# Kernel optimization log

Hardware: AMD Instinct MI355X
Metric: run time of the kernel (lower is better)

## Reference

```python
import jax, jax.numpy as jnp
import numpy as np

HEADS = 8
DIM_HEAD = 64
WINDOW = 128
PERSIST = 4
EPS = 1.1920929e-07  # torch nn.RMSNorm default eps = finfo(fp32).eps


def _rope_freqs(n, d, dtype):
    inv_freq = 1.0 / (10000.0 ** (jnp.arange(0, d, 2, dtype=jnp.float32) / d))
    freqs = jnp.arange(n, dtype=jnp.float32)[:, None] * inv_freq[None, :]  # [n, d/2]
    freqs = jnp.repeat(freqs, 2, axis=-1)  # interleaved repeat -> [n, d]
    return jnp.cos(freqs).astype(dtype), jnp.sin(freqs).astype(dtype)


def _rotate_half(x):
    # interleaved pairs (x0,x1),(x2,x3)... -> (-x1,x0),(-x3,x2)...
    x = x.reshape(*x.shape[:-1], -1, 2)
    x1, x2 = x[..., 0], x[..., 1]
    return jnp.stack((-x2, x1), axis=-1).reshape(*x.shape[:-2], -1)


def setup_inputs() -> dict:
    key = jax.random.key(0)
    k1, k2, k3 = jax.random.split(key, 3)
    B, N, D = 1, 4096, 1024
    dim_inner = HEADS * DIM_HEAD  # 512
    return {
        "seq": jax.random.normal(k1, (B, N, D), dtype=jnp.float32),
        "g": jnp.ones((D,), dtype=jnp.float32),
        "w_qkv": jax.random.normal(k2, (D, 3 * dim_inner), dtype=jnp.float32) * 0.02,
        "w_out": jax.random.normal(k3, (dim_inner, D), dtype=jnp.float32) * 0.02,
    }


def reference(seq, g, w_qkv, w_out):
    B, N, D = seq.shape
    H, Dh = HEADS, DIM_HEAD

    # RMSNorm
    x = seq * jax.lax.rsqrt(jnp.mean(seq * seq, axis=-1, keepdims=True) + EPS) * g

    # QKV projection -> [B, H, N, Dh]
    qkv = x @ w_qkv
    q, k, v = jnp.split(qkv, 3, axis=-1)
    to_heads = lambda t: t.reshape(B, N, H, Dh).transpose(0, 2, 1, 3)
    q, k, v = map(to_heads, (q, k, v))

    # rotary embeddings (same positions for q and k)
    cos, sin = _rope_freqs(N, Dh, q.dtype)
    q = q * cos + _rotate_half(q) * sin
    k = k * cos + _rotate_half(k) * sin

    # causal & (persist | sliding-window) mask
    idx = jnp.arange(N)
    dist = idx[:, None] - idx[None, :]
    mask = (dist >= 0) & ((idx[None, :] < PERSIST) | (dist <= WINDOW))  # [N, N]

    scale = Dh ** -0.5
    scores = jnp.einsum("bhid,bhjd->bhij", q, k) * scale
    neg = -jnp.finfo(scores.dtype).max
    scores = jnp.where(mask[None, None], scores, neg)
    attn = jax.nn.softmax(scores, axis=-1)
    out = jnp.einsum("bhij,bhjd->bhid", attn, v)

    out = out.transpose(0, 2, 1, 3).reshape(B, N, H * Dh)
    return out @ w_out
```

## Files before the change

### kernel.cpp

```cpp
#include <hip/hip_runtime.h>
#include <hip/hip_bf16.h>
#include <math.h>

#define SEQ    4096
#define DMODEL 1024
#define NHEADS 8
#define DH     64
#define DINNER 512
#define NQKV   1536
#define WINDOW 128
#define PERSIST 4
#define EPS 1.1920929e-07f

typedef unsigned short u16;
typedef unsigned int   u32;
typedef __bf16  bf16_8 __attribute__((ext_vector_type(8)));
typedef float   f32x4  __attribute__((ext_vector_type(4)));

union BV { bf16_8 v; u16 s[8]; };

__device__ __forceinline__ float b2f(u16 u) {
    union { u32 i; float f; } v; v.i = ((u32)u) << 16; return v.f;
}
__device__ __forceinline__ u16 f2b(float f) {
    union { float f; u32 i; } v; v.f = f;
    u32 i = v.i;
    u32 r = (i + 0x7fffu + ((i >> 16) & 1u)) >> 16;
    return (u16)r;
}

#define GLD16(gp, lp) __builtin_amdgcn_global_load_lds( \
    (const __attribute__((address_space(1))) void*)(gp), \
    (__attribute__((address_space(3))) void*)(lp), 16, 0, 0)

__device__ __forceinline__ void transpose_tile(const float* __restrict__ src,
                                               u16* __restrict__ dst,
                                               int K, int N, int bn, int bk,
                                               u16 (*t)[65], int tid) {
    int r = tid >> 4, c4 = (tid & 15) * 4;
    #pragma unroll
    for (int it = 0; it < 4; it++) {
        int row = r + it * 16;
        float4 v = *(const float4*)(src + (size_t)(bk + row) * N + bn + c4);
        t[row][c4 + 0] = f2b(v.x);
        t[row][c4 + 1] = f2b(v.y);
        t[row][c4 + 2] = f2b(v.z);
        t[row][c4 + 3] = f2b(v.w);
    }
    __syncthreads();
    #pragma unroll
    for (int it = 0; it < 4; it++) {
        int n = r + it * 16;
        u16* d = dst + (size_t)(bn + n) * K + bk + c4;
        d[0] = t[c4 + 0][n];
        d[1] = t[c4 + 1][n];
        d[2] = t[c4 + 2][n];
        d[3] = t[c4 + 3][n];
    }
}

__global__ __launch_bounds__(256) void prep_kernel(const float* __restrict__ wqkv,
                                                   const float* __restrict__ wout,
                                                   const float* __restrict__ seq,
                                                   const float* __restrict__ g,
                                                   u16* __restrict__ wqkv_bt,
                                                   u16* __restrict__ wout_bt,
                                                   u16* __restrict__ x) {
    __shared__ u16 t[64][65];
    __shared__ float wsum[4];
    int b = blockIdx.x, tid = threadIdx.x;
    if (b < 384) {
        transpose_tile(wqkv, wqkv_bt, DMODEL, NQKV, (b % 24) * 64, (b / 24) * 64, t, tid);
    } else if (b < 512) {
        int bb = b - 384;
        transpose_tile(wout, wout_bt, DINNER, DMODEL, (bb % 16) * 64, (bb / 16) * 64, t, tid);
    } else {
        int row = b - 512;
        float4 v = *(const float4*)(seq + (size_t)row * DMODEL + tid * 4);
        float ss = v.x*v.x + v.y*v.y + v.z*v.z + v.w*v.w;
        #pragma unroll
        for (int o = 32; o > 0; o >>= 1) ss += __shfl_xor(ss, o);
        if ((tid & 63) == 0) wsum[tid >> 6] = ss;
        __syncthreads();
        float tot = wsum[0] + wsum[1] + wsum[2] + wsum[3];
        float rstd = rsqrtf(tot * (1.0f / DMODEL) + EPS);
        float4 gv = *(const float4*)(g + tid * 4);
        uint2 o;
        o.x = (u32)f2b(v.x * rstd * gv.x) | ((u32)f2b(v.y * rstd * gv.y) << 16);
        o.y = (u32)f2b(v.z * rstd * gv.z) | ((u32)f2b(v.w * rstd * gv.w) << 16);
        *(uint2*)(x + (size_t)row * DMODEL + tid * 4) = o;
    }
}

template <int MODE>
__global__ __launch_bounds__(256, 3) void gemm4_kernel(const u16* __restrict__ A,
                                                       const u16* __restrict__ Bt,
                                                       u16* __restrict__ C0,
                                                       u16* __restrict__ C1,
                                                       u16* __restrict__ C2,
                                                       float* __restrict__ Cf,
                                                       int nbx, int M, int N, int K) {
    __shared__ u16 As[2][64 * 64];
    __shared__ u16 Bs[2][128 * 64];
    int b = blockIdx.x;
    int per = gridDim.x >> 3;
    int idx = (b & 7) * per + (b >> 3);
    int bx = idx % nbx, by = idx / nbx;
    int tid = threadIdx.x, lane = tid & 63, wave = tid >> 6;
    int m16 = lane & 15, quad = lane >> 4;
    int rw0 = (wave & 1) * 32, cw0 = (wave >> 1) * 64;

    f32x4 acc[2][4];
    #pragma unroll
    for (int mt = 0; mt < 2; mt++)
        #pragma unroll
        for (int nt = 0; nt < 4; nt++) acc[mt][nt] = (f32x4){0.f, 0.f, 0.f, 0.f};

    int lrow = lane & 7, lkc = lane >> 3;
    const u16* Ag = A  + (size_t)(by * 64  + lrow) * K + lkc * 8;
    const u16* Bg = Bt + (size_t)(bx * 128 + lrow) * K + lkc * 8;
    int niter = K >> 6;

    {
        #pragma unroll
        for (int r = 0; r < 2; r++) { int gg = wave * 2 + r; GLD16(Ag + (size_t)(gg * 8) * K, As[0] + gg * 512); }
        #pragma unroll
        for (int r = 0; r < 4; r++) { int gg = wave * 4 + r; GLD16(Bg + (size_t)(gg * 8) * K, Bs[0] + gg * 512); }
    }
    __syncthreads();

    for (int it = 0; it < niter; it++) {
        int cur = it & 1;
        if (it + 1 < niter) {
            int k0 = (it + 1) << 6;
            int nxt = cur ^ 1;
            #pragma unroll
            for (int r = 0; r < 2; r++) { int gg = wave * 2 + r; GLD16(Ag + (size_t)(gg * 8) * K + k0, As[nxt] + gg * 512); }
            #pragma unroll
            for (int r = 0; r < 4; r++) { int gg = wave * 4 + r; GLD16(Bg + (size_t)(gg * 8) * K + k0, Bs[nxt] + gg * 512); }
        }
        #pragma unroll
        for (int kk = 0; kk < 2; kk++) {
            int kc = kk * 4 + quad;
            bf16_8 afr[2], bfr[4];
            #pragma unroll
            for (int mt = 0; mt < 2; mt++) {
                int row = rw0 + mt * 16 + m16;
                afr[mt] = *(const bf16_8*)(As[cur] + (row >> 3) * 512 + kc * 64 + (row & 7) * 8);
            }
            #pragma unroll
            for (int nt = 0; nt < 4; nt++) {
                int col = cw0 + nt * 16 + m16;
                bfr[nt] = *(const bf16_8*)(Bs[cur] + (col >> 3) * 512 + kc * 64 + (col & 7) * 8);
            }
            #pragma unroll
            for (int mt = 0; mt < 2; mt++)
                #pragma unroll
                for (int nt = 0; nt < 4; nt++)
                    acc[mt][nt] = __builtin_amdgcn_mfma_f32_16x16x32_bf16(afr[mt], bfr[nt], acc[mt][nt], 0, 0, 0);
        }
        __syncthreads();
    }

    #pragma unroll
    for (int nt = 0; nt < 4; nt++) {
        int col = bx * 128 + cw0 + nt * 16 + m16;
        if (MODE == 0) {
            int tt = (col & 63) >> 1;
            float inv = exp2f(-(float)(2 * tt) * (13.287712379549449f / 64.0f));
            bool isv = (col >= 2 * DINNER);
            bool odd = (col & 1);
            int tens = col >> 9, hh = (col >> 6) & 7, dh = col & 63;
            u16* dst = (tens == 0) ? C0 : ((tens == 1) ? C1 : C2);
            #pragma unroll
            for (int mt = 0; mt < 2; mt++) {
                #pragma unroll
                for (int r = 0; r < 4; r++) {
                    int row = by * 64 + rw0 + mt * 16 + quad * 4 + r;
                    float own = acc[mt][nt][r];
                    float part = __shfl_xor(own, 1);
                    float val = own;
                    if (!isv) {
                        float s, c;
                        __sincosf((float)row * inv, &s, &c);
                        val = odd ? (own * c + part * s) : (own * c - part * s);
                    }
                    dst[((size_t)hh * SEQ + row) * DH + dh] = f2b(val);
                }
            }
        } else {
            #pragma unroll
            for (int mt = 0; mt < 2; mt++) {
                #pragma unroll
                for (int r = 0; r < 4; r++) {
                    int row = by * 64 + rw0 + mt * 16 + quad * 4 + r;
                    Cf[(size_t)row * N + col] = acc[mt][nt][r];
                }
            }
        }
    }
}

#define AROWS 208
#define KLD   72
#define PLD   168
#define VLD   222

__global__ __launch_bounds__(256, 2) void attn_mfma(const u16* __restrict__ Q,
                                                    const u16* __restrict__ Kt,
                                                    const u16* __restrict__ V,
                                                    u16* __restrict__ O) {
    __shared__ __align__(16) char smem[29952 + 64 * VLD * 2];
    u16* Ks = (u16*)smem;
    u16* Ps = (u16*)smem;
    u16* Vt = (u16*)(smem + 29952);
    int i0 = blockIdx.x * 64, h = blockIdx.y;
    int tid = threadIdx.x, wave = tid >> 6, lane = tid & 63;
    int m16 = lane & 15, quad = lane >> 4;
    int smin = (i0 > WINDOW) ? i0 - WINDOW : 0;

    for (int idx = tid; idx < AROWS * 8; idx += 256) {
        int row = idx >> 3, c = idx & 7;
        int j = (row < 16) ? row : (smin + row - 16);
        size_t goff = ((size_t)h * SEQ + j) * DH + c * 8;
        *(bf16_8*)(Ks + row * KLD + c * 8) = *(const bf16_8*)(Kt + goff);
        union BV u; u.v = *(const bf16_8*)(V + goff);
        #pragma unroll
        for (int e = 0; e < 8; e++) Vt[(c * 8 + e) * VLD + row] = u.s[e];
    }

    int iw0 = i0 + wave * 16;
    int iq = iw0 + m16;
    const u16* qrow = Q + ((size_t)h * SEQ + iq) * DH;
    bf16_8 qa = *(const bf16_8*)(qrow + quad * 8);
    bf16_8 qb = *(const bf16_8*)(qrow + 32 + quad * 8);
    __syncthreads();

    int start_w = (iw0 > WINDOW) ? iw0 - WINDOW : 0;
    int Dw = start_w - smin;
    int tlast = 31 + iw0 - start_w;
    int nch = (tlast >> 4) + 1;
    int nk32 = (tlast >> 5) + 1;

    f32x4 S[10];
    #pragma unroll
    for (int c = 0; c < 10; c++) {
        if (c < nch) {
            int t = c * 16 + m16;
            int row = (c == 0) ? t : (t + Dw);
            const u16* kp = Ks + row * KLD;
            bf16_8 kb0 = *(const bf16_8*)(kp + quad * 8);
            bf16_8 kb1 = *(const bf16_8*)(kp + 32 + quad * 8);
            f32x4 s = (f32x4){0.f, 0.f, 0.f, 0.f};
            s = __builtin_amdgcn_mfma_f32_16x16x32_bf16(qa, kb0, s, 0, 0, 0);
            s = __builtin_amdgcn_mfma_f32_16x16x32_bf16(qb, kb1, s, 0, 0, 0);
            S[c] = s;
        }
    }
    __syncthreads();

    float mrow[4] = {-1e30f, -1e30f, -1e30f, -1e30f};
    #pragma unroll
    for (int c = 0; c < 10; c++) {
        if (c < nch) {
            int t = c * 16 + m16;
            int j = (c == 0) ? t : (start_w + t - 16);
            #pragma unroll
            for (int r = 0; r < 4; r++) {
                int i = iw0 + quad * 4 + r;
                bool valid = (c == 0) ? (j < PERSIST && j < start_w)
                                      : (j <= i && (i - j <= WINDOW || j < PERSIST));
                float sv = valid ? S[c][r] * 0.125f : -1e30f;
                S[c][r] = sv;
                mrow[r] = fmaxf(mrow[r], sv);
            }
        }
    }
    #pragma unroll
    for (int r = 0; r < 4; r++) {
        #pragma unroll
        for (int o = 1; o < 16; o <<= 1) mrow[r] = fmaxf(mrow[r], __shfl_xor(mrow[r], o));
    }
    float srow[4] = {0.f, 0.f, 0.f, 0.f};
    #pragma unroll
    for (int c = 0; c < 10; c++) {
        if (c < nch) {
            #pragma unroll
            for (int r = 0; r < 4; r++) {
                float p = expf(S[c][r] - mrow[r]);
                S[c][r] = p;
                srow[r] += p;
            }
        }
    }
    #pragma unroll
    for (int r = 0; r < 4; r++) {
        #pragma unroll
        for (int o = 1; o < 16; o <<= 1) srow[r] += __shfl_xor(srow[r], o);
    }

    u16* pw = Ps + wave * 16 * PLD;
    #pragma unroll
    for (int c = 0; c < 10; c++) {
        #pragma unroll
        for (int r = 0; r < 4; r++) {
            u16 val = (c < nch) ? f2b(S[c][r]) : (u16)0;
            pw[(quad * 4 + r) * PLD + c * 16 + m16] = val;
        }
    }

    f32x4 oacc[4];
    #pragma unroll
    for (int nt = 0; nt < 4; nt++) oacc[nt] = (f32x4){0.f, 0.f, 0.f, 0.f};
    #pragma unroll
    for (int c2 = 0; c2 < 5; c2++) {
        if (c2 < nk32) {
            bf16_8 af = *(const bf16_8*)(pw + m16 * PLD + c2 * 32 + quad * 8);
            int kbase = c2 * 32 + quad * 8;
            int rowb = (kbase < 16) ? kbase : (kbase + Dw);
            #pragma unroll
            for (int nt = 0; nt < 4; nt++) {
                int d = nt * 16 + m16;
                bf16_8 bv = *(const bf16_8*)(Vt + d * VLD + rowb);
                oacc[nt] = __builtin_amdgcn_mfma_f32_16x16x32_bf16(af, bv, oacc[nt], 0, 0, 0);
            }
        }
    }

    #pragma unroll
    for (int nt = 0; nt < 4; nt++) {
        #pragma unroll
        for (int r = 0; r < 4; r++) {
            int i = iw0 + quad * 4 + r;
            O[(size_t)i * DINNER + h * DH + nt * 16 + m16] = f2b(oacc[nt][r] / srow[r]);
        }
    }
}

extern "C" void kernel_launch(void* const* d_in, const int* in_sizes, int n_in,
                              void* d_out, int out_size, void* d_ws, size_t ws_size,
                              hipStream_t stream) {
    const float* seq  = (const float*)d_in[0];
    const float* g    = (const float*)d_in[1];
    const float* wqkv = (const float*)d_in[2];
    const float* wout = (const float*)d_in[3];
    float* out = (float*)d_out;

    char* ws = (char*)d_ws;
    u16* x       = (u16*)(ws);
    u16* q       = (u16*)(ws + 8ll  * 1024 * 1024);
    u16* k       = (u16*)(ws + 12ll * 1024 * 1024);
    u16* v       = (u16*)(ws + 16ll * 1024 * 1024);
    u16* att     = (u16*)(ws + 20ll * 1024 * 1024);
    u16* wqkv_bt = (u16*)(ws + 24ll * 1024 * 1024);
    u16* wout_bt = (u16*)(ws + 27ll * 1024 * 1024);

    prep_kernel<<<4608, 256, 0, stream>>>(wqkv, wout, seq, g, wqkv_bt, wout_bt, x);

    gemm4_kernel<0><<<768, 256, 0, stream>>>(x, wqkv_bt, q, k, v, nullptr,
                                             NQKV / 128, SEQ, NQKV, DMODEL);

    dim3 g2(SEQ / 64, NHEADS);
    attn_mfma<<<g2, 256, 0, stream>>>(q, k, v, att);

    gemm4_kernel<1><<<512, 256, 0, stream>>>(att, wout_bt, nullptr, nullptr, nullptr, out,
                                             DMODEL / 128, SEQ, DMODEL, DINNER);
}
```

Measured before the change: 148.7 us.

## Load GEMM A fragments straight to registers and give each wave a 16x128 tile

After: 149.4 us. About the same (+0.5%).

```diff
diff --git a/kernel.cpp b/kernel.cpp
--- a/kernel.cpp
+++ b/kernel.cpp
@@ -93,14 +93,13 @@
 }
 
 template <int MODE>
-__global__ __launch_bounds__(256, 3) void gemm4_kernel(const u16* __restrict__ A,
+__global__ __launch_bounds__(256, 4) void gemm6_kernel(const u16* __restrict__ A,
                                                        const u16* __restrict__ Bt,
                                                        u16* __restrict__ C0,
                                                        u16* __restrict__ C1,
                                                        u16* __restrict__ C2,
                                                        float* __restrict__ Cf,
                                                        int nbx, int M, int N, int K) {
-    __shared__ u16 As[2][64 * 64];
     __shared__ u16 Bs[2][128 * 64];
     int b = blockIdx.x;
     int per = gridDim.x >> 3;
@@ -108,63 +107,56 @@
     int bx = idx % nbx, by = idx / nbx;
     int tid = threadIdx.x, lane = tid & 63, wave = tid >> 6;
     int m16 = lane & 15, quad = lane >> 4;
-    int rw0 = (wave & 1) * 32, cw0 = (wave >> 1) * 64;
-
-    f32x4 acc[2][4];
-    #pragma unroll
-    for (int mt = 0; mt < 2; mt++)
-        #pragma unroll
-        for (int nt = 0; nt < 4; nt++) acc[mt][nt] = (f32x4){0.f, 0.f, 0.f, 0.f};
-
+
+    f32x4 acc[8];
+    #pragma unroll
+    for (int nt = 0; nt < 8; nt++) acc[nt] = (f32x4){0.f, 0.f, 0.f, 0.f};
+
+    const u16* Arow = A + (size_t)(by * 64 + wave * 16 + m16) * K + quad * 8;
     int lrow = lane & 7, lkc = lane >> 3;
-    const u16* Ag = A  + (size_t)(by * 64  + lrow) * K + lkc * 8;
     const u16* Bg = Bt + (size_t)(bx * 128 + lrow) * K + lkc * 8;
     int niter = K >> 6;
 
-    {
-        #pragma unroll
-        for (int r = 0; r < 2; r++) { int gg = wave * 2 + r; GLD16(Ag + (size_t)(gg * 8) * K, As[0] + gg * 512); }
-        #pragma unroll
-        for (int r = 0; r < 4; r++) { int gg = wave * 4 + r; GLD16(Bg + (size_t)(gg * 8) * K, Bs[0] + gg * 512); }
-    }
+    #pragma unroll
+    for (int r = 0; r < 4; r++) {
+        int gg = wave * 4 + r;
+        GLD16(Bg + (size_t)(gg * 8) * K, Bs[0] + gg * 512);
+    }
+    bf16_8 acur0 = *(const bf16_8*)(Arow);
+    bf16_8 acur1 = *(const bf16_8*)(Arow + 32);
     __syncthreads();
 
     for (int it = 0; it < niter; it++) {
         int cur = it & 1;
+        bf16_8 anxt0, anxt1;
         if (it + 1 < niter) {
             int k0 = (it + 1) << 6;
-            int nxt = cur ^ 1;
-            #pragma unroll
-            for (int r = 0; r < 2; r++) { int gg = wave * 2 + r; GLD16(Ag + (size_t)(gg * 8) * K + k0, As[nxt] + gg * 512); }
-            #pragma unroll
-            for (int r = 0; r < 4; r++) { int gg = wave * 4 + r; GLD16(Bg + (size_t)(gg * 8) * K + k0, Bs[nxt] + gg * 512); }
+            #pragma unroll
+            for (int r = 0; r < 4; r++) {
+                int gg = wave * 4 + r;
+                GLD16(Bg + (size_t)(gg * 8) * K + k0, Bs[cur ^ 1] + gg * 512);
+            }
+            anxt0 = *(const bf16_8*)(Arow + k0);
+            anxt1 = *(const bf16_8*)(Arow + k0 + 32);
         }
         #pragma unroll
         for (int kk = 0; kk < 2; kk++) {
+            bf16_8 af = kk ? acur1 : acur0;
             int kc = kk * 4 + quad;
-            bf16_8 afr[2], bfr[4];
-            #pragma unroll
-            for (int mt = 0; mt < 2; mt++) {
-                int row = rw0 + mt * 16 + m16;
-                afr[mt] = *(const bf16_8*)(As[cur] + (row >> 3) * 512 + kc * 64 + (row & 7) * 8);
-            }
-            #pragma unroll
-            for (int nt = 0; nt < 4; nt++) {
-                int col = cw0 + nt * 16 + m16;
-                bfr[nt] = *(const bf16_8*)(Bs[cur] + (col >> 3) * 512 + kc * 64 + (col & 7) * 8);
-            }
-            #pragma unroll
-            for (int mt = 0; mt < 2; mt++)
-                #pragma unroll
-                for (int nt = 0; nt < 4; nt++)
-                    acc[mt][nt] = __builtin_amdgcn_mfma_f32_16x16x32_bf16(afr[mt], bfr[nt], acc[mt][nt], 0, 0, 0);
-        }
+            #pragma unroll
+            for (int nt = 0; nt < 8; nt++) {
+                int col = nt * 16 + m16;
+                bf16_8 bf = *(const bf16_8*)(Bs[cur] + (col >> 3) * 512 + kc * 64 + (col & 7) * 8);
+                acc[nt] = __builtin_amdgcn_mfma_f32_16x16x32_bf16(af, bf, acc[nt], 0, 0, 0);
+            }
+        }
+        acur0 = anxt0; acur1 = anxt1;
         __syncthreads();
     }
 
     #pragma unroll
-    for (int nt = 0; nt < 4; nt++) {
-        int col = bx * 128 + cw0 + nt * 16 + m16;
+    for (int nt = 0; nt < 8; nt++) {
+        int col = bx * 128 + nt * 16 + m16;
         if (MODE == 0) {
             int tt = (col & 63) >> 1;
             float inv = exp2f(-(float)(2 * tt) * (13.287712379549449f / 64.0f));
@@ -173,29 +165,23 @@
             int tens = col >> 9, hh = (col >> 6) & 7, dh = col & 63;
             u16* dst = (tens == 0) ? C0 : ((tens == 1) ? C1 : C2);
             #pragma unroll
-            for (int mt = 0; mt < 2; mt++) {
-                #pragma unroll
-                for (int r = 0; r < 4; r++) {
-                    int row = by * 64 + rw0 + mt * 16 + quad * 4 + r;
-                    float own = acc[mt][nt][r];
-                    float part = __shfl_xor(own, 1);
-                    float val = own;
-                    if (!isv) {
-                        float s, c;
-                        __sincosf((float)row * inv, &s, &c);
-                        val = odd ? (own * c + part * s) : (own * c - part * s);
-                    }
-                    dst[((size_t)hh * SEQ + row) * DH + dh] = f2b(val);
+            for (int r = 0; r < 4; r++) {
+                int row = by * 64 + wave * 16 + quad * 4 + r;
+                float own = acc[nt][r];
+                float part = __shfl_xor(own, 1);
+                float val = own;
+                if (!isv) {
+                    float s, c;
+                    __sincosf((float)row * inv, &s, &c);
+                    val = odd ? (own * c + part * s) : (own * c - part * s);
                 }
+                dst[((size_t)hh * SEQ + row) * DH + dh] = f2b(val);
             }
         } else {
             #pragma unroll
-            for (int mt = 0; mt < 2; mt++) {
-                #pragma unroll
-                for (int r = 0; r < 4; r++) {
-                    int row = by * 64 + rw0 + mt * 16 + quad * 4 + r;
-                    Cf[(size_t)row * N + col] = acc[mt][nt][r];
-                }
+            for (int r = 0; r < 4; r++) {
+                int row = by * 64 + wave * 16 + quad * 4 + r;
+                Cf[(size_t)row * N + col] = acc[nt][r];
             }
         }
     }
@@ -357,12 +343,12 @@
 
     prep_kernel<<<4608, 256, 0, stream>>>(wqkv, wout, seq, g, wqkv_bt, wout_bt, x);
 
-    gemm4_kernel<0><<<768, 256, 0, stream>>>(x, wqkv_bt, q, k, v, nullptr,
+    gemm6_kernel<0><<<768, 256, 0, stream>>>(x, wqkv_bt, q, k, v, nullptr,
                                              NQKV / 128, SEQ, NQKV, DMODEL);
 
     dim3 g2(SEQ / 64, NHEADS);
     attn_mfma<<<g2, 256, 0, stream>>>(q, k, v, att);
 
-    gemm4_kernel<1><<<512, 256, 0, stream>>>(att, wout_bt, nullptr, nullptr, nullptr, out,
+    gemm6_kernel<1><<<512, 256, 0, stream>>>(att, wout_bt, nullptr, nullptr, nullptr, out,
                                              DMODEL / 128, SEQ, DMODEL, DINNER);
 }
```
